# Kernel optimization log

Hardware: AMD Instinct MI355X
Metric: run time of the kernel (lower is better)

## Reference

```python
import jax, jax.numpy as jnp
import numpy as np

B, IN, H, G, WR = 8192, 1024, 1024, 2, 64
UR = [64, 64]


def setup_inputs() -> dict:
    key = jax.random.key(0)
    ks = jax.random.split(key, 9)
    hg = H // G
    return {
        "x": jax.random.normal(ks[0], (B, IN), jnp.float32),
        "h": jax.random.normal(ks[1], (B, H), jnp.float32),
        "c": jax.random.normal(ks[2], (B, H), jnp.float32),
        "u_x": 0.1 * jax.random.normal(ks[3], (IN, WR), jnp.float32),
        "v_x": 0.1 * jax.random.normal(ks[4], (4 * H, WR), jnp.float32),
        "u_h_0": 0.1 * jax.random.normal(ks[5], (G, hg, UR[0]), jnp.float32),
        "v_h_0": 0.1 * jax.random.normal(ks[6], (G, UR[0], 4 * hg), jnp.float32),
        "u_h_1": 0.1 * jax.random.normal(ks[7], (G, hg, UR[1]), jnp.float32),
        "v_h_1": 0.1 * jax.random.normal(ks[8], (G, UR[1], 4 * hg), jnp.float32),
        "bias_x": jnp.ones((1, 4 * H), jnp.float32),
        "bias_h": jnp.ones((1, 4 * H), jnp.float32),
    }


def reference(x, h, c, u_x, v_x, u_h_0, v_h_0, u_h_1, v_h_1, bias_x, bias_h):
    b = h.shape[0]
    hg = H // G
    # input-to-hidden low-rank projection: [B, 4H]
    gx = (x @ u_x) @ v_x.T + bias_x
    xf, xi, xn, xo = jnp.split(gx, 4, axis=1)  # each [B, H]

    hv = h.reshape(b, G, hg)  # [B, G, H/G]
    u_hs = [u_h_0, u_h_1]
    v_hs = [v_h_0, v_h_1]
    acc = None
    for i in range(G):
        # torch code rotates the group index list cumulatively each step:
        # step i uses permutation roll(arange(G), -i)
        perm = np.roll(np.arange(G), -i)
        h_op = hv[:, perm, :]  # [B, G, hg]
        t = jnp.einsum('bgd,gdr->bgr', h_op, u_hs[i])  # [B, G, r_i]
        t = jnp.einsum('bgr,grk->bgk', t, v_hs[i])     # [B, G, 4hg]
        acc = t if acc is None else acc + t

    # chunk along last dim into 4 gates, flatten group dim -> [B, H]
    f_h, i_h, n_h, o_h = [p.reshape(b, H) for p in jnp.split(acc, 4, axis=2)]
    hf, hi, hn, ho = jnp.split(bias_h, 4, axis=1)

    inputgate = jax.nn.sigmoid(xi + hi + i_h)
    forgetgate = jax.nn.sigmoid(xf + hf + f_h)
    outputgate = jax.nn.sigmoid(xo + ho + o_h)
    newgate = jnp.tanh(xn + hn + n_h)
    c_next = forgetgate * c + inputgate * newgate
    h_next = outputgate * jnp.tanh(c_next)
    return (h_next, c_next)
```

## Files before the change

kernel.cpp:

```cpp
#include <hip/hip_runtime.h>
#include <hip/hip_bf16.h>


typedef __bf16 bf16_t;
typedef __bf16 bf16x4 __attribute__((ext_vector_type(4)));
typedef __bf16 bf16x8 __attribute__((ext_vector_type(8)));
typedef float f32x4 __attribute__((ext_vector_type(4)));

#define MFMA16x16x32(a, b, c) __builtin_amdgcn_mfma_f32_16x16x32_bf16((a), (b), (c), 0, 0, 0)

#define TA_OFF 0
#define BX_OFF 5242880
#define BH_OFF 5373952
#define BW_OFF 5636096

__device__ inline float fast_sigmoid(float x) {
  return __builtin_amdgcn_rcpf(1.f + __expf(-x));
}
__device__ inline float fast_tanh(float x) {
  return 2.f * __builtin_amdgcn_rcpf(1.f + __expf(-2.f * x)) - 1.f;
}

__global__ __launch_bounds__(256) void prep_kernel(
    const float* __restrict__ u_x, const float* __restrict__ u_h_0,
    const float* __restrict__ u_h_1, const float* __restrict__ v_h_0,
    const float* __restrict__ v_h_1, const float* __restrict__ v_x,
    bf16_t* __restrict__ Bx, bf16_t* __restrict__ Bh,
    bf16_t* __restrict__ Bw) {
  int t = blockIdx.x * 256 + threadIdx.x;
  int lane = t & 63;
  int lo = lane & 15, quad = lane >> 4;
  if (t < 8192) {
    int kk = (t >> 6) & 31, tt = t >> 11;
    int k0 = kk * 32 + quad * 8;
    const float* src = u_x + 16 * tt + lo;
    bf16x8 v;
#pragma unroll
    for (int j = 0; j < 8; ++j) v[j] = (bf16_t)src[(size_t)(k0 + j) * 64];
    *(bf16x8*)(Bx + (size_t)t * 8) = v;
  } else if (t < 24576) {
    int o2 = t - 8192;
    int kk = (o2 >> 6) & 15, sub = (o2 >> 10) & 3, s = o2 >> 12;
    int d0 = kk * 32 + quad * 8;
    const float* src =
        ((s & 1) ? u_h_1 : u_h_0) + (size_t)(s >> 1) * 32768 + 16 * sub + lo;
    bf16x8 v;
#pragma unroll
    for (int j = 0; j < 8; ++j) v[j] = (bf16_t)src[(size_t)(d0 + j) * 64];
    *(bf16x8*)(Bh + (size_t)o2 * 8) = v;
  } else {
    int t3 = t - 24576;
    int chunk = t3 >> 6;
    int ks = chunk % 6, rowt = chunk / 6;
    int gq = rowt >> 3, nt = rowt & 7;
    int gg = gq >> 4, qt = gq & 15;
    int row = 16 * nt + lo;
    int w = row >> 5, ql = row & 31;
    int k0 = ks * 32 + quad * 8;
    int m = gg * 512 + qt * 32 + ql;
    int q = qt * 32 + ql;
    bf16x8 v;
    if (ks < 2) {
      const float4* p = (const float4*)(v_x + (size_t)(w * 1024 + m) * 64 + k0);
      float4 va = p[0], vb = p[1];
      v[0] = (bf16_t)va.x; v[1] = (bf16_t)va.y;
      v[2] = (bf16_t)va.z; v[3] = (bf16_t)va.w;
      v[4] = (bf16_t)vb.x; v[5] = (bf16_t)vb.y;
      v[6] = (bf16_t)vb.z; v[7] = (bf16_t)vb.w;
    } else if (ks < 4) {
      const float* src = v_h_0 + (size_t)gg * 131072 +
                         (size_t)(k0 - 64) * 2048 + w * 512 + q;
#pragma unroll
      for (int j = 0; j < 8; ++j) v[j] = (bf16_t)src[(size_t)j * 2048];
    } else {
      const float* src = v_h_1 + (size_t)gg * 131072 +
                         (size_t)(k0 - 128) * 2048 + w * 512 + q;
#pragma unroll
      for (int j = 0; j < 8; ++j) v[j] = (bf16_t)src[(size_t)j * 2048];
    }
    *(bf16x8*)(Bw + (size_t)t3 * 8) = v;
  }
}

__global__ __launch_bounds__(512) void phase1_kernel(
    const float* __restrict__ x, const float* __restrict__ h,
    const bf16_t* __restrict__ Bx, const bf16_t* __restrict__ Bh,
    bf16_t* __restrict__ TA) {
  __shared__ bf16_t z[16][2072];
  __shared__ bf16_t pre[16][328];
  const int b0 = blockIdx.x * 16;
  const int tid = threadIdx.x;
  const int wv = tid >> 6, lane = tid & 63;
  const int lo = lane & 15, quad = lane >> 4;
  const int srow = tid >> 5, sc = tid & 31;

  {
    const float* srcx = x + (size_t)(b0 + srow) * 1024 + sc * 4;
    const float* srch = h + (size_t)(b0 + srow) * 1024 + sc * 4;
#pragma unroll
    for (int j = 0; j < 8; ++j) {
      float4 v = *(const float4*)(srcx + j * 128);
      bf16x4 pk;
      pk[0] = (bf16_t)v.x; pk[1] = (bf16_t)v.y;
      pk[2] = (bf16_t)v.z; pk[3] = (bf16_t)v.w;
      *(bf16x4*)&z[srow][sc * 4 + j * 128] = pk;
    }
#pragma unroll
    for (int j = 0; j < 8; ++j) {
      float4 v = *(const float4*)(srch + j * 128);
      bf16x4 pk;
      pk[0] = (bf16_t)v.x; pk[1] = (bf16_t)v.y;
      pk[2] = (bf16_t)v.z; pk[3] = (bf16_t)v.w;
      *(bf16x4*)&z[srow][1024 + sc * 4 + j * 128] = pk;
    }
  }
  __syncthreads();

  if (wv < 4) {
    f32x4 accx = {0.f, 0.f, 0.f, 0.f};
    const bf16_t* bx = Bx + ((size_t)(wv * 32) * 64 + lane) * 8;
    for (int kk = 0; kk < 32; ++kk) {
      bf16x8 af = *(const bf16x8*)&z[lo][kk * 32 + quad * 8];
      bf16x8 bfr = *(const bf16x8*)(bx + (size_t)kk * 512);
      accx = MFMA16x16x32(af, bfr, accx);
    }
#pragma unroll
    for (int r = 0; r < 4; ++r) pre[quad * 4 + r][16 * wv + lo] = (bf16_t)accx[r];

    const int u = 12 + wv;
    f32x4 acch = {0.f, 0.f, 0.f, 0.f};
    const bf16_t* bh = Bh + ((size_t)(u * 16) * 64 + lane) * 8;
    for (int kk = 0; kk < 16; ++kk) {
      bf16x8 af = *(const bf16x8*)&z[lo][1024 + kk * 32 + quad * 8];
      bf16x8 bfr = *(const bf16x8*)(bh + (size_t)kk * 512);
      acch = MFMA16x16x32(af, bfr, acch);
    }
#pragma unroll
    for (int r = 0; r < 4; ++r)
      pre[quad * 4 + r][64 + u * 16 + lo] = (bf16_t)acch[r];
  } else {
    const int ub = (wv - 4) * 3;
    f32x4 acc[3];
#pragma unroll
    for (int i = 0; i < 3; ++i) acc[i] = (f32x4){0.f, 0.f, 0.f, 0.f};
    int hoffA[3];
#pragma unroll
    for (int i = 0; i < 3; ++i) {
      int s = (ub + i) >> 2;
      hoffA[i] = 1024 + ((s == 1 || s == 2) ? 512 : 0);
    }
    const bf16_t* bh = Bh + ((size_t)(ub * 16) * 64 + lane) * 8;
    for (int kk = 0; kk < 16; ++kk) {
#pragma unroll
      for (int i = 0; i < 3; ++i) {
        bf16x8 af = *(const bf16x8*)&z[lo][hoffA[i] + kk * 32 + quad * 8];
        bf16x8 bfr = *(const bf16x8*)(bh + ((size_t)i * 16 + kk) * 512);
        acc[i] = MFMA16x16x32(af, bfr, acc[i]);
      }
    }
#pragma unroll
    for (int i = 0; i < 3; ++i)
#pragma unroll
      for (int r = 0; r < 4; ++r)
        pre[quad * 4 + r][64 + (ub + i) * 16 + lo] = (bf16_t)acc[i][r];
  }
  __syncthreads();

#pragma unroll
  for (int it = 0; it < 2; ++it) {
    int slot = it * 512 + tid;
    if (slot < 640) {
      int cc = slot >> 6, ln = slot & 63;
      int llo = ln & 15, lq = ln >> 4;
      bf16x8 v = *(const bf16x8*)&pre[llo][cc * 32 + lq * 8];
      *(bf16x8*)(TA + (((size_t)blockIdx.x * 10 + cc) * 64 + ln) * 8) = v;
    }
  }
}

__global__ __launch_bounds__(512, 4) void phase2_kernel(
    const bf16_t* __restrict__ TA, const bf16_t* __restrict__ Bw,
    const float* __restrict__ bias_x, const float* __restrict__ bias_h,
    const float* __restrict__ c, float* __restrict__ out) {
  __shared__ bf16_t bs[3072 * 8];

  const int b0 = blockIdx.x * 256;
  const int gq = blockIdx.y;
  const int g = gq >> 4, qt = gq & 15;
  const int tid = threadIdx.x;
  const int wv = tid >> 6, lane = tid & 63;
  const int lo = lane & 15, quad = lane >> 4;

  bf16x8 a[2][6];
#pragma unroll
  for (int mt = 0; mt < 2; ++mt) {
    int rt = blockIdx.x * 16 + wv * 2 + mt;
#pragma unroll
    for (int ks = 0; ks < 6; ++ks) {
      int cc = (ks < 2) ? ks : (g * 4 + ks);
      a[mt][ks] = *(const bf16x8*)(TA + (((size_t)rt * 10 + cc) * 64 + lane) * 8);
    }
  }

  {
    const bf16_t* src = Bw + (size_t)gq * 24576;
#pragma unroll
    for (int cch = 0; cch < 6; ++cch) {
      int ch = cch * 512 + tid;
      *(bf16x8*)&bs[(size_t)ch * 8] = *(const bf16x8*)(src + (size_t)ch * 8);
    }
  }

  float cin[2][4][2];
#pragma unroll
  for (int mt = 0; mt < 2; ++mt)
#pragma unroll
    for (int r = 0; r < 4; ++r) {
      int b = b0 + wv * 32 + mt * 16 + quad * 4 + r;
#pragma unroll
      for (int cq = 0; cq < 2; ++cq) {
        int m = g * 512 + qt * 32 + cq * 16 + lo;
        cin[mt][r][cq] = c[(size_t)b * 1024 + m];
      }
    }
  float bsum[4][2];
#pragma unroll
  for (int w = 0; w < 4; ++w)
#pragma unroll
    for (int cq = 0; cq < 2; ++cq) {
      int n = w * 1024 + g * 512 + qt * 32 + cq * 16 + lo;
      bsum[w][cq] = bias_x[n] + bias_h[n];
    }
  __syncthreads();

  f32x4 acc[2][8];
#pragma unroll
  for (int mt = 0; mt < 2; ++mt)
#pragma unroll
    for (int nt = 0; nt < 8; ++nt) acc[mt][nt] = (f32x4){0.f, 0.f, 0.f, 0.f};

#pragma unroll
  for (int nt = 0; nt < 8; ++nt) {
#pragma unroll
    for (int ks = 0; ks < 6; ++ks) {
      bf16x8 bfr = *(const bf16x8*)&bs[(size_t)(((nt * 6 + ks) << 6) + lane) * 8];
      acc[0][nt] = MFMA16x16x32(a[0][ks], bfr, acc[0][nt]);
      acc[1][nt] = MFMA16x16x32(a[1][ks], bfr, acc[1][nt]);
    }
  }

#pragma unroll
  for (int mt = 0; mt < 2; ++mt)
#pragma unroll
    for (int r = 0; r < 4; ++r) {
      int b = b0 + wv * 32 + mt * 16 + quad * 4 + r;
#pragma unroll
      for (int cq = 0; cq < 2; ++cq) {
        int m = g * 512 + qt * 32 + cq * 16 + lo;
        float fv = acc[mt][0 + cq][r] + bsum[0][cq];
        float iv = acc[mt][2 + cq][r] + bsum[1][cq];
        float nv = acc[mt][4 + cq][r] + bsum[2][cq];
        float ov = acc[mt][6 + cq][r] + bsum[3][cq];
        float ig = fast_sigmoid(iv);
        float fg = fast_sigmoid(fv);
        float og = fast_sigmoid(ov);
        float ng = fast_tanh(nv);
        float cn = fg * cin[mt][r][cq] + ig * ng;
        float hn = og * fast_tanh(cn);
        out[(size_t)b * 1024 + m] = hn;
        out[8388608ull + (size_t)b * 1024 + m] = cn;
      }
    }
}

extern "C" void kernel_launch(void* const* d_in, const int* in_sizes, int n_in,
                              void* d_out, int out_size, void* d_ws,
                              size_t ws_size, hipStream_t stream) {
  const float* x = (const float*)d_in[0];
  const float* h = (const float*)d_in[1];
  const float* c = (const float*)d_in[2];
  const float* u_x = (const float*)d_in[3];
  const float* v_x = (const float*)d_in[4];
  const float* u_h_0 = (const float*)d_in[5];
  const float* v_h_0 = (const float*)d_in[6];
  const float* u_h_1 = (const float*)d_in[7];
  const float* v_h_1 = (const float*)d_in[8];
  const float* bias_x = (const float*)d_in[9];
  const float* bias_h = (const float*)d_in[10];

  char* ws = (char*)d_ws;
  bf16_t* TA = (bf16_t*)(ws + TA_OFF);
  bf16_t* Bx = (bf16_t*)(ws + BX_OFF);
  bf16_t* Bh = (bf16_t*)(ws + BH_OFF);
  bf16_t* Bw = (bf16_t*)(ws + BW_OFF);

  prep_kernel<<<480, 256, 0, stream>>>(u_x, u_h_0, u_h_1, v_h_0, v_h_1, v_x,
                                       Bx, Bh, Bw);
  phase1_kernel<<<512, 512, 0, stream>>>(x, h, Bx, Bh, TA);
  phase2_kernel<<<dim3(32, 32), 512, 0, stream>>>(TA, Bw, bias_x, bias_h, c,
                                                  (float*)d_out);
}
```

Before: 218.6 us.

## Make phase2 persistent over batch tiles with register prefetch of next tile

```diff
diff --git a/kernel.cpp b/kernel.cpp
--- a/kernel.cpp
+++ b/kernel.cpp
@@ -178,51 +178,27 @@
   }
 }
 
-__global__ __launch_bounds__(512, 4) void phase2_kernel(
+__global__ __launch_bounds__(256, 2) void phase2_kernel(
     const bf16_t* __restrict__ TA, const bf16_t* __restrict__ Bw,
     const float* __restrict__ bias_x, const float* __restrict__ bias_h,
     const float* __restrict__ c, float* __restrict__ out) {
   __shared__ bf16_t bs[3072 * 8];
 
-  const int b0 = blockIdx.x * 256;
   const int gq = blockIdx.y;
   const int g = gq >> 4, qt = gq & 15;
   const int tid = threadIdx.x;
   const int wv = tid >> 6, lane = tid & 63;
   const int lo = lane & 15, quad = lane >> 4;
 
-  bf16x8 a[2][6];
-#pragma unroll
-  for (int mt = 0; mt < 2; ++mt) {
-    int rt = blockIdx.x * 16 + wv * 2 + mt;
-#pragma unroll
-    for (int ks = 0; ks < 6; ++ks) {
-      int cc = (ks < 2) ? ks : (g * 4 + ks);
-      a[mt][ks] = *(const bf16x8*)(TA + (((size_t)rt * 10 + cc) * 64 + lane) * 8);
-    }
-  }
-
   {
     const bf16_t* src = Bw + (size_t)gq * 24576;
 #pragma unroll
-    for (int cch = 0; cch < 6; ++cch) {
-      int ch = cch * 512 + tid;
+    for (int cch = 0; cch < 12; ++cch) {
+      int ch = cch * 256 + tid;
       *(bf16x8*)&bs[(size_t)ch * 8] = *(const bf16x8*)(src + (size_t)ch * 8);
     }
   }
 
-  float cin[2][4][2];
-#pragma unroll
-  for (int mt = 0; mt < 2; ++mt)
-#pragma unroll
-    for (int r = 0; r < 4; ++r) {
-      int b = b0 + wv * 32 + mt * 16 + quad * 4 + r;
-#pragma unroll
-      for (int cq = 0; cq < 2; ++cq) {
-        int m = g * 512 + qt * 32 + cq * 16 + lo;
-        cin[mt][r][cq] = c[(size_t)b * 1024 + m];
-      }
-    }
   float bsum[4][2];
 #pragma unroll
   for (int w = 0; w < 4; ++w)
@@ -231,46 +207,120 @@
       int n = w * 1024 + g * 512 + qt * 32 + cq * 16 + lo;
       bsum[w][cq] = bias_x[n] + bias_h[n];
     }
+
+  bf16x8 a[2][6];
+  float cin[2][4][2];
+  {
+    const int bt = blockIdx.x;
+#pragma unroll
+    for (int mt = 0; mt < 2; ++mt) {
+      int rt = bt * 8 + wv * 2 + mt;
+#pragma unroll
+      for (int ks = 0; ks < 6; ++ks) {
+        int cc = (ks < 2) ? ks : (g * 4 + ks);
+        a[mt][ks] =
+            *(const bf16x8*)(TA + (((size_t)rt * 10 + cc) * 64 + lane) * 8);
+      }
+    }
+    const int b0 = bt * 128;
+#pragma unroll
+    for (int mt = 0; mt < 2; ++mt)
+#pragma unroll
+      for (int r = 0; r < 4; ++r) {
+        int b = b0 + wv * 32 + mt * 16 + quad * 4 + r;
+#pragma unroll
+        for (int cq = 0; cq < 2; ++cq) {
+          int m = g * 512 + qt * 32 + cq * 16 + lo;
+          cin[mt][r][cq] = c[(size_t)b * 1024 + m];
+        }
+      }
+  }
   __syncthreads();
 
-  f32x4 acc[2][8];
-#pragma unroll
-  for (int mt = 0; mt < 2; ++mt)
-#pragma unroll
-    for (int nt = 0; nt < 8; ++nt) acc[mt][nt] = (f32x4){0.f, 0.f, 0.f, 0.f};
-
-#pragma unroll
-  for (int nt = 0; nt < 8; ++nt) {
-#pragma unroll
-    for (int ks = 0; ks < 6; ++ks) {
-      bf16x8 bfr = *(const bf16x8*)&bs[(size_t)(((nt * 6 + ks) << 6) + lane) * 8];
-      acc[0][nt] = MFMA16x16x32(a[0][ks], bfr, acc[0][nt]);
-      acc[1][nt] = MFMA16x16x32(a[1][ks], bfr, acc[1][nt]);
-    }
-  }
-
-#pragma unroll
-  for (int mt = 0; mt < 2; ++mt)
-#pragma unroll
-    for (int r = 0; r < 4; ++r) {
-      int b = b0 + wv * 32 + mt * 16 + quad * 4 + r;
-#pragma unroll
-      for (int cq = 0; cq < 2; ++cq) {
-        int m = g * 512 + qt * 32 + cq * 16 + lo;
-        float fv = acc[mt][0 + cq][r] + bsum[0][cq];
-        float iv = acc[mt][2 + cq][r] + bsum[1][cq];
-        float nv = acc[mt][4 + cq][r] + bsum[2][cq];
-        float ov = acc[mt][6 + cq][r] + bsum[3][cq];
-        float ig = fast_sigmoid(iv);
-        float fg = fast_sigmoid(fv);
-        float og = fast_sigmoid(ov);
-        float ng = fast_tanh(nv);
-        float cn = fg * cin[mt][r][cq] + ig * ng;
-        float hn = og * fast_tanh(cn);
-        out[(size_t)b * 1024 + m] = hn;
-        out[8388608ull + (size_t)b * 1024 + m] = cn;
-      }
-    }
+#pragma unroll 1
+  for (int it = 0; it < 4; ++it) {
+    const int bt = blockIdx.x + it * 16;
+    const int b0 = bt * 128;
+
+    f32x4 acc[2][8];
+#pragma unroll
+    for (int mt = 0; mt < 2; ++mt)
+#pragma unroll
+      for (int nt = 0; nt < 8; ++nt) acc[mt][nt] = (f32x4){0.f, 0.f, 0.f, 0.f};
+
+#pragma unroll
+    for (int nt = 0; nt < 8; ++nt) {
+#pragma unroll
+      for (int ks = 0; ks < 6; ++ks) {
+        bf16x8 bfr =
+            *(const bf16x8*)&bs[(size_t)(((nt * 6 + ks) << 6) + lane) * 8];
+        acc[0][nt] = MFMA16x16x32(a[0][ks], bfr, acc[0][nt]);
+        acc[1][nt] = MFMA16x16x32(a[1][ks], bfr, acc[1][nt]);
+      }
+    }
+
+    bf16x8 an[2][6];
+    float cinn[2][4][2];
+    if (it < 3) {
+      const int btn = blockIdx.x + (it + 1) * 16;
+#pragma unroll
+      for (int mt = 0; mt < 2; ++mt) {
+        int rt = btn * 8 + wv * 2 + mt;
+#pragma unroll
+        for (int ks = 0; ks < 6; ++ks) {
+          int cc = (ks < 2) ? ks : (g * 4 + ks);
+          an[mt][ks] =
+              *(const bf16x8*)(TA + (((size_t)rt * 10 + cc) * 64 + lane) * 8);
+        }
+      }
+      const int b0n = btn * 128;
+#pragma unroll
+      for (int mt = 0; mt < 2; ++mt)
+#pragma unroll
+        for (int r = 0; r < 4; ++r) {
+          int b = b0n + wv * 32 + mt * 16 + quad * 4 + r;
+#pragma unroll
+          for (int cq = 0; cq < 2; ++cq) {
+            int m = g * 512 + qt * 32 + cq * 16 + lo;
+            cinn[mt][r][cq] = c[(size_t)b * 1024 + m];
+          }
+        }
+    }
+
+#pragma unroll
+    for (int mt = 0; mt < 2; ++mt)
+#pragma unroll
+      for (int r = 0; r < 4; ++r) {
+        int b = b0 + wv * 32 + mt * 16 + quad * 4 + r;
+#pragma unroll
+        for (int cq = 0; cq < 2; ++cq) {
+          int m = g * 512 + qt * 32 + cq * 16 + lo;
+          float fv = acc[mt][0 + cq][r] + bsum[0][cq];
+          float iv = acc[mt][2 + cq][r] + bsum[1][cq];
+          float nv = acc[mt][4 + cq][r] + bsum[2][cq];
+          float ov = acc[mt][6 + cq][r] + bsum[3][cq];
+          float ig = fast_sigmoid(iv);
+          float fg = fast_sigmoid(fv);
+          float og = fast_sigmoid(ov);
+          float ng = fast_tanh(nv);
+          float cn = fg * cin[mt][r][cq] + ig * ng;
+          float hn = og * fast_tanh(cn);
+          out[(size_t)b * 1024 + m] = hn;
+          out[8388608ull + (size_t)b * 1024 + m] = cn;
+        }
+      }
+
+#pragma unroll
+    for (int mt = 0; mt < 2; ++mt)
+#pragma unroll
+      for (int ks = 0; ks < 6; ++ks) a[mt][ks] = an[mt][ks];
+#pragma unroll
+    for (int mt = 0; mt < 2; ++mt)
+#pragma unroll
+      for (int r = 0; r < 4; ++r)
+#pragma unroll
+        for (int cq = 0; cq < 2; ++cq) cin[mt][r][cq] = cinn[mt][r][cq];
+  }
 }
 
 extern "C" void kernel_launch(void* const* d_in, const int* in_sizes, int n_in,
@@ -297,6 +347,6 @@
   prep_kernel<<<480, 256, 0, stream>>>(u_x, u_h_0, u_h_1, v_h_0, v_h_1, v_x,
                                        Bx, Bh, Bw);
   phase1_kernel<<<512, 512, 0, stream>>>(x, h, Bx, Bh, TA);
-  phase2_kernel<<<dim3(32, 32), 512, 0, stream>>>(TA, Bw, bias_x, bias_h, c,
+  phase2_kernel<<<dim3(16, 32), 256, 0, stream>>>(TA, Bw, bias_x, bias_h, c,
                                                   (float*)d_out);
 }
```

Result: slower. 260.4 us (+19.2%).
